# Optimization experiments

Hardware: AMD Instinct MI355X
Metric: run time of the kernel (lower is better)

The kernel has to match this reference:

```python
import jax, jax.numpy as jnp
import numpy as np

D = 128          # hidden_dim
H = 4            # num attention heads (torch default nhead=4 in this module)
DH = D // H
NA = 4096        # author nodes
NP = 100000      # paper nodes
EAP = 500000     # author->paper edges
EPA = 500000     # paper->author edges
DFF = 2048       # TransformerEncoderLayer FFN dim (torch default)
OUT = 16
IN_A = 128
IN_P = 256
EPS = 1e-5


def layer_norm(x, g, b):
    mu = jnp.mean(x, -1, keepdims=True)
    var = jnp.mean((x - mu) ** 2, -1, keepdims=True)
    return (x - mu) / jnp.sqrt(var + EPS) * g + b


def scatter_mean(vals, idx, n):
    # torch_scatter 'mean': empty segments yield 0
    s = jax.ops.segment_sum(vals, idx, num_segments=n)
    c = jax.ops.segment_sum(jnp.ones((vals.shape[0], 1), vals.dtype), idx, num_segments=n)
    return s / jnp.maximum(c, 1.0)


def metapath_layer(x_src, x_dst, src, dst, Wv, bv, Wo, bo, g, b):
    # nn.MultiheadAttention applied per-edge with seq_len=1 (query/key/value are
    # [1, E, D]); softmax over a single key is identically 1, so the attention
    # output is exactly out_proj(v_proj(x_src[src])) -- q/k projections have no
    # effect on the output (and zero gradient).
    v = x_src[src] @ Wv.T + bv            # [E, D] gather + value projection
    attn = v @ Wo.T + bo                  # output projection
    agg = scatter_mean(attn, dst, x_dst.shape[0])
    return layer_norm(agg + x_dst, g, b)


def fusion_layer(x, Wqkv, bqkv, Wo, bo, W1, b1, W2, b2, g1, bt1, g2, bt2):
    # torch TransformerEncoderLayer defaults: post-norm, relu, batch_first=False,
    # so x: [S=NA (seq), M (batch = #metapaths), D].
    S, M, _ = x.shape
    qkv = x @ Wqkv.T + bqkv               # [S, M, 3D]
    q, k, v = jnp.split(qkv, 3, axis=-1)
    q = q.reshape(S, M, H, DH)
    k = k.reshape(S, M, H, DH)
    v = v.reshape(S, M, H, DH)
    scores = jnp.einsum('smhd,tmhd->mhst', q, k) / np.float32(np.sqrt(DH))
    a = jax.nn.softmax(scores, axis=-1)
    ctx = jnp.einsum('mhst,tmhd->smhd', a, v).reshape(S, M, D)
    x = layer_norm(x + ctx @ Wo.T + bo, g1, bt1)
    ff = jax.nn.relu(x @ W1.T + b1) @ W2.T + b2
    return layer_norm(x + ff, g2, bt2)


def setup_inputs() -> dict:
    key = jax.random.key(0)
    ks = iter(jax.random.split(key, 64))
    def nrm(shape, scale=0.02):
        return jax.random.normal(next(ks), shape, dtype=jnp.float32) * scale
    inp = {
        'x_author': jax.random.normal(next(ks), (NA, IN_A), dtype=jnp.float32),
        'x_paper': jax.random.normal(next(ks), (NP, IN_P), dtype=jnp.float32),
        'src_ap': jax.random.randint(next(ks), (EAP,), 0, NA),
        'dst_ap': jax.random.randint(next(ks), (EAP,), 0, NP),
        'src_pa': jax.random.randint(next(ks), (EPA,), 0, NP),
        'dst_pa': jax.random.randint(next(ks), (EPA,), 0, NA),
        'pa_W': nrm((D, IN_A)), 'pa_b': nrm((D,)),
        'pp_W': nrm((D, IN_P)), 'pp_b': nrm((D,)),
        'f_Wqkv': nrm((3 * D, D)), 'f_bqkv': nrm((3 * D,)),
        'f_Wo': nrm((D, D)), 'f_bo': nrm((D,)),
        'f_W1': nrm((DFF, D)), 'f_b1': nrm((DFF,)),
        'f_W2': nrm((D, DFF)), 'f_b2': nrm((D,)),
        'f_g1': jnp.ones((D,), jnp.float32), 'f_bt1': jnp.zeros((D,), jnp.float32),
        'f_g2': jnp.ones((D,), jnp.float32), 'f_bt2': jnp.zeros((D,), jnp.float32),
        'cls_W': nrm((OUT, D)), 'cls_b': nrm((OUT,)),
    }
    for i in range(3):
        inp[f'l{i}_Wv'] = nrm((D, D)); inp[f'l{i}_bv'] = nrm((D,))
        inp[f'l{i}_Wo'] = nrm((D, D)); inp[f'l{i}_bo'] = nrm((D,))
        inp[f'l{i}_g'] = jnp.ones((D,), jnp.float32); inp[f'l{i}_b'] = jnp.zeros((D,), jnp.float32)
    return inp


def reference(x_author, x_paper, src_ap, dst_ap, src_pa, dst_pa,
              pa_W, pa_b, pp_W, pp_b,
              f_Wqkv, f_bqkv, f_Wo, f_bo, f_W1, f_b1, f_W2, f_b2,
              f_g1, f_bt1, f_g2, f_bt2, cls_W, cls_b,
              l0_Wv, l0_bv, l0_Wo, l0_bo, l0_g, l0_b,
              l1_Wv, l1_bv, l1_Wo, l1_bo, l1_g, l1_b,
              l2_Wv, l2_bv, l2_Wo, l2_bo, l2_g, l2_b):
    # project node features to hidden_dim
    ha = x_author @ pa_W.T + pa_b         # [NA, D]
    hp = x_paper @ pp_W.T + pp_b          # [NP, D]
    # metapath 0: paper -> author (one MetapathLayer)
    mp0 = metapath_layer(hp, ha, src_pa, dst_pa, l0_Wv, l0_bv, l0_Wo, l0_bo, l0_g, l0_b)
    # metapath 1: author -> paper -> author (two MetapathLayers)
    t = metapath_layer(ha, hp, src_ap, dst_ap, l1_Wv, l1_bv, l1_Wo, l1_bo, l1_g, l1_b)
    mp1 = metapath_layer(t, ha, src_pa, dst_pa, l2_Wv, l2_bv, l2_Wo, l2_bo, l2_g, l2_b)
    stacked = jnp.stack([mp0, mp1], axis=1)   # [NA, 2, D]
    fused = fusion_layer(stacked, f_Wqkv, f_bqkv, f_Wo, f_bo,
                         f_W1, f_b1, f_W2, f_b2,
                         f_g1, f_bt1, f_g2, f_bt2).mean(axis=1)
    return fused @ cls_W.T + cls_b            # [NA, OUT]
```

## Files before the change

kernel.cpp:

```cpp
#include <hip/hip_runtime.h>
#include <math.h>

constexpr int NA = 4096, NP = 100000, E_AP = 500000, E_PA = 500000;
constexpr int D = 128, DFF = 2048, NOUT = 16, IN_A = 128, IN_P = 256;

typedef __attribute__((ext_vector_type(8))) short bf16x8;
typedef __attribute__((ext_vector_type(4))) float f32x4;
typedef unsigned int u32;

__device__ __forceinline__ ushort f2b(float x) {
    union { float f; unsigned u; } v; v.f = x;
    unsigned r = v.u + 0x7fff + ((v.u >> 16) & 1);
    return (ushort)(r >> 16);
}
__device__ __forceinline__ float b2f(ushort h) {
    union { unsigned u; float f; } v; v.u = (unsigned)h << 16;
    return v.f;
}
__device__ __forceinline__ u32 fbits(float x) {
    union { float f; u32 u; } v; v.f = x; return v.u;
}

__device__ __forceinline__ bf16x8 cvtfrag(float4 a, float4 b) {
    union { u32 w[4]; bf16x8 v; } r;
    asm("v_cvt_pk_bf16_f32 %0, %1, %2" : "=v"(r.w[0]) : "v"(a.x), "v"(a.y));
    asm("v_cvt_pk_bf16_f32 %0, %1, %2" : "=v"(r.w[1]) : "v"(a.z), "v"(a.w));
    asm("v_cvt_pk_bf16_f32 %0, %1, %2" : "=v"(r.w[2]) : "v"(b.x), "v"(b.y));
    asm("v_cvt_pk_bf16_f32 %0, %1, %2" : "=v"(r.w[3]) : "v"(b.z), "v"(b.w));
    return r.v;
}

#define GLL(gp, lp) __builtin_amdgcn_global_load_lds( \
    (const __attribute__((address_space(1))) u32*)(gp), \
    (__attribute__((address_space(3))) u32*)(lp), 16, 0, 0)

#define MFMA16(a, b, c) __builtin_amdgcn_mfma_f32_16x16x32_bf16((a), (b), (c), 0, 0, 0)

__global__ __launch_bounds__(256) void gemm_bf16(
    const ushort* __restrict__ Abf, const float* __restrict__ Af32, int lda,
    const ushort* __restrict__ B, int ldb,
    const float* __restrict__ bias,
    float* __restrict__ outf, ushort* __restrict__ outh, int ldc,
    int M, int N, int K, int act)
{
    __shared__ uint8_t lds[(16 + 32) * 1040];
    uint8_t* sAb = lds;
    uint8_t* sBb = lds + 16 * 1040;

    const int wave = threadIdx.x >> 6;
    const int lane = threadIdx.x & 63;
    const int l16 = lane & 15, quad = lane >> 4;
    const int row0 = blockIdx.y * 64;
    const int col0 = blockIdx.x * 128;
    const int wrg = (wave >> 1) * 2;
    const int wc0 = (wave & 1) * 64;
    const int nz = gridDim.z;
    const int ksub = K / nz;
    const int kbeg = blockIdx.z * ksub;
    const int kgrps = ksub >> 7;

    f32x4 acc[2][4] = {};

    const int sr = lane & 15, sc = lane >> 4;
    const int arow = min(row0 + lane, M - 1);
    const int ag = lane >> 4;
    uint8_t* adst = sAb + (ag * 4 + wave) * 1040 + sr * 16;

    for (int grp = 0; grp < kgrps; ++grp) {
        const int kg = kbeg + grp * 128;
        if (grp) __syncthreads();
        #pragma unroll
        for (int gg = 0; gg < 2; ++gg) {
            int g = wave * 2 + gg;
            const ushort* bp = B + (long)(col0 + g * 16 + sr) * ldb + kg + sc * 8;
            #pragma unroll
            for (int s = 0; s < 4; ++s)
                GLL(bp + s * 32, sBb + (g * 4 + s) * 1040);
        }
        if (Af32) {
            const float* ap = Af32 + (long)arow * lda + kg + wave * 32;
            #pragma unroll
            for (int q = 0; q < 4; ++q) {
                float4 f0 = *(const float4*)(ap + q * 8);
                float4 f1 = *(const float4*)(ap + q * 8 + 4);
                *(bf16x8*)(adst + q * 256) = cvtfrag(f0, f1);
            }
        } else {
            const ushort* ap = Abf + (long)arow * lda + kg + wave * 32;
            #pragma unroll
            for (int q = 0; q < 4; ++q)
                *(bf16x8*)(adst + q * 256) = *(const bf16x8*)(ap + q * 8);
        }
        __syncthreads();
        #pragma unroll
        for (int s = 0; s < 4; ++s) {
            bf16x8 af[2], bfr[4];
            #pragma unroll
            for (int i = 0; i < 2; ++i)
                af[i] = *(const bf16x8*)(sAb + ((wrg + i) * 4 + s) * 1040 + lane * 16);
            #pragma unroll
            for (int j = 0; j < 4; ++j)
                bfr[j] = *(const bf16x8*)(sBb + (((wc0 >> 4) + j) * 4 + s) * 1040 + lane * 16);
            #pragma unroll
            for (int i = 0; i < 2; ++i)
                #pragma unroll
                for (int j = 0; j < 4; ++j)
                    acc[i][j] = MFMA16(af[i], bfr[j], acc[i][j]);
        }
    }

    if (outh && nz == 1) {
        __syncthreads();
        ushort* sC = (ushort*)lds;
        #pragma unroll
        for (int i = 0; i < 2; ++i) {
            #pragma unroll
            for (int r = 0; r < 4; ++r) {
                int lrow = wrg * 16 + i * 16 + quad * 4 + r;
                #pragma unroll
                for (int j = 0; j < 4; ++j) {
                    int lcol = wc0 + j * 16 + l16;
                    float v = acc[i][j][r] + (bias ? bias[col0 + lcol] : 0.f);
                    if (act) v = fmaxf(v, 0.f);
                    sC[lrow * 134 + lcol] = f2b(v);
                }
            }
        }
        __syncthreads();
        int rr = threadIdx.x >> 2, qq = threadIdx.x & 3;
        int grow = row0 + rr;
        if (grow < M) {
            const ushort* src = sC + rr * 134 + qq * 32;
            ushort* dst = outh + (long)grow * ldc + col0 + qq * 32;
            #pragma unroll
            for (int k = 0; k < 4; ++k)
                *(bf16x8*)(dst + k * 8) = *(const bf16x8*)(src + k * 8);
        }
        return;
    }

    #pragma unroll
    for (int i = 0; i < 2; ++i) {
        #pragma unroll
        for (int r = 0; r < 4; ++r) {
            int row = row0 + wrg * 16 + i * 16 + quad * 4 + r;
            if (row >= M) continue;
            #pragma unroll
            for (int j = 0; j < 4; ++j) {
                int col = col0 + wc0 + j * 16 + l16;
                if (nz > 1) {
                    atomicAdd(&outf[(long)row * ldc + col], acc[i][j][r]);
                } else {
                    float v = acc[i][j][r] + (bias ? bias[col] : 0.f);
                    if (act) v = fmaxf(v, 0.f);
                    if (outf) outf[(long)row * ldc + col] = v;
                }
            }
        }
    }
}

__global__ __launch_bounds__(256) void ffn_fused(
    const ushort* __restrict__ x1b,
    const ushort* __restrict__ W1b,
    const ushort* __restrict__ W2b,
    const float* __restrict__ b1,
    float* __restrict__ outf)
{
    __shared__ uint8_t lds[56 * 1040];
    uint8_t* sX  = lds;
    uint8_t* sW1 = lds + 16 * 1040;
    uint8_t* sW2 = lds + 32 * 1040;
    uint8_t* sH  = lds + 48 * 1040;

    const int wave = threadIdx.x >> 6;
    const int lane = threadIdx.x & 63;
    const int l16 = lane & 15, quad = lane >> 4;
    const int sr = lane & 15, sc = lane >> 4;
    const int row0 = blockIdx.x * 64;
    const int dbeg = blockIdx.y * 512;

    const int xg = wave >> 1;
    const int ch = wave & 1;

    {
        const ushort* xp = x1b + (long)(row0 + wave * 16 + sr) * 128 + sc * 8;
        #pragma unroll
        for (int s = 0; s < 4; ++s)
            GLL(xp + s * 32, sX + (wave * 4 + s) * 1040);
    }

    f32x4 acc2[2][4] = {};

    for (int c = 0; c < 8; ++c) {
        const int kc = dbeg + c * 64;
        {
            const ushort* w1p = W1b + (long)(kc + wave * 16 + sr) * 128 + sc * 8;
            #pragma unroll
            for (int s = 0; s < 4; ++s)
                GLL(w1p + s * 32, sW1 + (wave * 4 + s) * 1040);
            #pragma unroll
            for (int gg = 0; gg < 2; ++gg) {
                int cg = wave * 2 + gg;
                const ushort* w2p = W2b + (long)(cg * 16 + sr) * 2048 + kc + sc * 8;
                #pragma unroll
                for (int s2 = 0; s2 < 2; ++s2)
                    GLL(w2p + s2 * 32, sW2 + (cg * 2 + s2) * 1040);
            }
        }
        __syncthreads();

        f32x4 acc1[2][2] = {};
        #pragma unroll
        for (int s = 0; s < 4; ++s) {
            bf16x8 a0 = *(const bf16x8*)(sX + ((xg * 2 + 0) * 4 + s) * 1040 + lane * 16);
            bf16x8 a1 = *(const bf16x8*)(sX + ((xg * 2 + 1) * 4 + s) * 1040 + lane * 16);
            bf16x8 w0 = *(const bf16x8*)(sW1 + ((ch * 2 + 0) * 4 + s) * 1040 + lane * 16);
            bf16x8 w1 = *(const bf16x8*)(sW1 + ((ch * 2 + 1) * 4 + s) * 1040 + lane * 16);
            acc1[0][0] = MFMA16(a0, w0, acc1[0][0]);
            acc1[0][1] = MFMA16(a0, w1, acc1[0][1]);
            acc1[1][0] = MFMA16(a1, w0, acc1[1][0]);
            acc1[1][1] = MFMA16(a1, w1, acc1[1][1]);
        }
        float bb0 = b1[kc + ch * 32 + l16];
        float bb1 = b1[kc + ch * 32 + 16 + l16];
        #pragma unroll
        for (int i = 0; i < 2; ++i) {
            uint8_t* hb = sH + ((xg * 2 + i) * 2 + ch) * 1040;
            #pragma unroll
            for (int j = 0; j < 2; ++j) {
                float bb = j ? bb1 : bb0;
                int q = ((j * 16 + l16) >> 3) & 3;
                int byo = (l16 & 7) * 2;
                #pragma unroll
                for (int r = 0; r < 4; ++r) {
                    float v = fmaxf(acc1[i][j][r] + bb, 0.f);
                    *(ushort*)(hb + q * 256 + (quad * 4 + r) * 16 + byo) = f2b(v);
                }
            }
        }
        __syncthreads();

        #pragma unroll
        for (int s2 = 0; s2 < 2; ++s2) {
            bf16x8 h0 = *(const bf16x8*)(sH + ((xg * 2 + 0) * 2 + s2) * 1040 + lane * 16);
            bf16x8 h1 = *(const bf16x8*)(sH + ((xg * 2 + 1) * 2 + s2) * 1040 + lane * 16);
            #pragma unroll
            for (int j2 = 0; j2 < 4; ++j2) {
                bf16x8 wb = *(const bf16x8*)(sW2 + ((ch * 4 + j2) * 2 + s2) * 1040 + lane * 16);
                acc2[0][j2] = MFMA16(h0, wb, acc2[0][j2]);
                acc2[1][j2] = MFMA16(h1, wb, acc2[1][j2]);
            }
        }
        __syncthreads();
    }

    #pragma unroll
    for (int i = 0; i < 2; ++i)
        #pragma unroll
        for (int r = 0; r < 4; ++r) {
            int row = row0 + xg * 32 + i * 16 + quad * 4 + r;
            #pragma unroll
            for (int j2 = 0; j2 < 4; ++j2) {
                int col = ch * 64 + j2 * 16 + l16;
                atomicAdd(&outf[(long)row * 128 + col], acc2[i][j2][r]);
            }
        }
}

__global__ __launch_bounds__(256) void fuse_weights(
    const float* __restrict__ Wv0, const float* __restrict__ bv0,
    const float* __restrict__ Wo0, const float* __restrict__ bo0,
    const float* __restrict__ Wv1, const float* __restrict__ bv1,
    const float* __restrict__ Wo1, const float* __restrict__ bo1,
    const float* __restrict__ Wv2, const float* __restrict__ bv2,
    const float* __restrict__ Wo2, const float* __restrict__ bo2,
    ushort* __restrict__ Wfb, float* __restrict__ beff)
{
    int blk = blockIdx.x;
    if (blk >= 192) {
        int l = blk - 192;
        const float* bv = l == 0 ? bv0 : (l == 1 ? bv1 : bv2);
        const float* Wo = l == 0 ? Wo0 : (l == 1 ? Wo1 : Wo2);
        const float* bo = l == 0 ? bo0 : (l == 1 ? bo1 : bo2);
        if (threadIdx.x < 128) {
            int r = threadIdx.x;
            float acc = bo[r];
            #pragma unroll 8
            for (int j = 0; j < 128; ++j) acc += Wo[r * 128 + j] * bv[j];
            beff[l * 128 + r] = acc;
        }
        return;
    }
    int l = blk >> 6;
    const float* Wv = l == 0 ? Wv0 : (l == 1 ? Wv1 : Wv2);
    const float* Wo = l == 0 ? Wo0 : (l == 1 ? Wo1 : Wo2);
    int r = (blk & 63) * 2 + (threadIdx.x >> 7);
    int c = threadIdx.x & 127;
    float acc = 0.f;
    #pragma unroll 8
    for (int j = 0; j < 128; ++j)
        acc += Wo[r * 128 + j] * Wv[j * 128 + c];
    Wfb[l * 16384 + r * 128 + c] = f2b(acc);
}

__global__ void hist2(const int* __restrict__ dA, int* __restrict__ cA,
                      const int* __restrict__ dP, int* __restrict__ cP, int E)
{
    int e = blockIdx.x * 256 + threadIdx.x;
    if (e >= E) return;
    if (blockIdx.y == 0) atomicAdd(&cA[dA[e]], 1);
    else                 atomicAdd(&cP[dP[e]], 1);
}

__global__ __launch_bounds__(256) void scan_local2(
    const int* __restrict__ inA, int* __restrict__ outA, int* __restrict__ bsumA, int nA,
    const int* __restrict__ inP, int* __restrict__ outP, int* __restrict__ bsumP, int nP)
{
    const int* in  = blockIdx.y ? inP  : inA;
    int* out       = blockIdx.y ? outP : outA;
    int* bsum      = blockIdx.y ? bsumP : bsumA;
    int n          = blockIdx.y ? nP : nA;
    __shared__ int wsum[4];
    int t = threadIdx.x;
    int base = blockIdx.x * 1024 + t * 4;
    int v0 = (base + 0 < n) ? in[base + 0] : 0;
    int v1 = (base + 1 < n) ? in[base + 1] : 0;
    int v2 = (base + 2 < n) ? in[base + 2] : 0;
    int v3 = (base + 3 < n) ? in[base + 3] : 0;
    int tsum = v0 + v1 + v2 + v3;
    int lane = t & 63;
    int x = tsum;
    #pragma unroll
    for (int o = 1; o < 64; o <<= 1) {
        int y = __shfl_up(x, o, 64);
        if (lane >= o) x += y;
    }
    int wid = t >> 6;
    if (lane == 63) wsum[wid] = x;
    __syncthreads();
    int woff = 0;
    #pragma unroll
    for (int ww = 0; ww < 3; ++ww) if (ww < wid) woff += wsum[ww];
    int excl = x - tsum + woff;
    if (base + 0 < n) out[base + 0] = excl;
    if (base + 1 < n) out[base + 1] = excl + v0;
    if (base + 2 < n) out[base + 2] = excl + v0 + v1;
    if (base + 3 < n) out[base + 3] = excl + v0 + v1 + v2;
    if (bsum && t == 255) bsum[blockIdx.x] = excl + tsum;
}

__global__ void scan_add2(int* __restrict__ offA, const int* __restrict__ bA,
                          int* __restrict__ curA, int nA,
                          int* __restrict__ offP, const int* __restrict__ bP,
                          int* __restrict__ curP, int nP)
{
    int* off       = blockIdx.y ? offP : offA;
    const int* bofs= blockIdx.y ? bP   : bA;
    int* cur       = blockIdx.y ? curP : curA;
    int n          = blockIdx.y ? nP : nA;
    int i = blockIdx.x * 256 + threadIdx.x;
    if (i < n) {
        int v = off[i] + bofs[i >> 10];
        off[i] = v;
        cur[i] = v;
    }
}

__global__ void fill2(const int* __restrict__ sA, const int* __restrict__ dA,
                      int* __restrict__ cuA, int* __restrict__ eA,
                      const int* __restrict__ sP, const int* __restrict__ dP,
                      int* __restrict__ cuP, int* __restrict__ eP, int E)
{
    int e = blockIdx.x * 256 + threadIdx.x;
    if (e >= E) return;
    if (blockIdx.y == 0) { int slot = atomicAdd(&cuA[dA[e]], 1); eA[slot] = sA[e]; }
    else                 { int slot = atomicAdd(&cuP[dP[e]], 1); eP[slot] = sP[e]; }
}

__global__ __launch_bounds__(256) void gather_sum(
    const ushort* __restrict__ z, const int* __restrict__ off,
    const int* __restrict__ cnt, const int* __restrict__ esrc,
    float* __restrict__ outf, int R)
{
    int grp = threadIdx.x >> 5;
    int tg  = threadIdx.x & 31;
    int gid = blockIdx.x * 8 + grp;
    int row = gid >> 2, chunk = gid & 3;
    if (row >= R) return;
    int e0 = off[row], deg = cnt[row];
    int c0 = e0 + (int)(((long)deg * chunk) >> 2);
    int c1 = e0 + (int)(((long)deg * (chunk + 1)) >> 2);
    if (c0 >= c1) return;
    float a0 = 0.f, a1 = 0.f, a2 = 0.f, a3 = 0.f;
    int e = c0;
    for (; e + 4 <= c1; e += 4) {
        int s0 = esrc[e], s1 = esrc[e + 1], s2 = esrc[e + 2], s3 = esrc[e + 3];
        ushort4 v0 = ((const ushort4*)(z + (long)s0 * 128))[tg];
        ushort4 v1 = ((const ushort4*)(z + (long)s1 * 128))[tg];
        ushort4 v2 = ((const ushort4*)(z + (long)s2 * 128))[tg];
        ushort4 v3 = ((const ushort4*)(z + (long)s3 * 128))[tg];
        a0 += b2f(v0.x) + b2f(v1.x) + b2f(v2.x) + b2f(v3.x);
        a1 += b2f(v0.y) + b2f(v1.y) + b2f(v2.y) + b2f(v3.y);
        a2 += b2f(v0.z) + b2f(v1.z) + b2f(v2.z) + b2f(v3.z);
        a3 += b2f(v0.w) + b2f(v1.w) + b2f(v2.w) + b2f(v3.w);
    }
    for (; e < c1; ++e) {
        int s = esrc[e];
        ushort4 v = ((const ushort4*)(z + (long)s * 128))[tg];
        a0 += b2f(v.x); a1 += b2f(v.y); a2 += b2f(v.z); a3 += b2f(v.w);
    }
    float* op = outf + (long)row * 128 + tg * 4;
    atomicAdd(op + 0, a0); atomicAdd(op + 1, a1);
    atomicAdd(op + 2, a2); atomicAdd(op + 3, a3);
}

__global__ __launch_bounds__(256) void gather_mean_ln(
    const ushort* __restrict__ z, const int* __restrict__ off,
    const int* __restrict__ cnt, const int* __restrict__ esrc,
    const ushort* __restrict__ base, const float* __restrict__ g,
    const float* __restrict__ b, ushort* __restrict__ outh, int R)
{
    int grp = threadIdx.x >> 5;
    int tg  = threadIdx.x & 31;
    int row = blockIdx.x * 8 + grp;
    if (row >= R) return;
    int e0 = off[row], deg = cnt[row];
    int eend = e0 + deg;
    float a0 = 0.f, a1 = 0.f, a2 = 0.f, a3 = 0.f;
    int e = e0;
    for (; e + 4 <= eend; e += 4) {
        int s0 = esrc[e], s1 = esrc[e + 1], s2 = esrc[e + 2], s3 = esrc[e + 3];
        ushort4 v0 = ((const ushort4*)(z + (long)s0 * 128))[tg];
        ushort4 v1 = ((const ushort4*)(z + (long)s1 * 128))[tg];
        ushort4 v2 = ((const ushort4*)(z + (long)s2 * 128))[tg];
        ushort4 v3 = ((const ushort4*)(z + (long)s3 * 128))[tg];
        a0 += b2f(v0.x) + b2f(v1.x) + b2f(v2.x) + b2f(v3.x);
        a1 += b2f(v0.y) + b2f(v1.y) + b2f(v2.y) + b2f(v3.y);
        a2 += b2f(v0.z) + b2f(v1.z) + b2f(v2.z) + b2f(v3.z);
        a3 += b2f(v0.w) + b2f(v1.w) + b2f(v2.w) + b2f(v3.w);
    }
    for (; e < eend; ++e) {
        int s = esrc[e];
        ushort4 v = ((const ushort4*)(z + (long)s * 128))[tg];
        a0 += b2f(v.x); a1 += b2f(v.y); a2 += b2f(v.z); a3 += b2f(v.w);
    }
    float inv = 1.f / fmaxf((float)deg, 1.f);
    ushort4 bs = ((const ushort4*)(base + (long)row * 128))[tg];
    float x0 = a0 * inv + b2f(bs.x), x1 = a1 * inv + b2f(bs.y);
    float x2 = a2 * inv + b2f(bs.z), x3 = a3 * inv + b2f(bs.w);
    float s1 = x0 + x1 + x2 + x3;
    #pragma unroll
    for (int o = 1; o < 32; o <<= 1) s1 += __shfl_xor(s1, o, 64);
    float mu = s1 * (1.f / 128.f);
    float d0 = x0 - mu, d1 = x1 - mu, d2 = x2 - mu, d3 = x3 - mu;
    float s2 = d0 * d0 + d1 * d1 + d2 * d2 + d3 * d3;
    #pragma unroll
    for (int o = 1; o < 32; o <<= 1) s2 += __shfl_xor(s2, o, 64);
    float rstd = rsqrtf(s2 * (1.f / 128.f) + 1e-5f);
    float4 gv = ((const float4*)g)[tg];
    float4 bv = ((const float4*)b)[tg];
    ushort4 h4;
    h4.x = f2b(d0 * rstd * gv.x + bv.x);
    h4.y = f2b(d1 * rstd * gv.y + bv.y);
    h4.z = f2b(d2 * rstd * gv.z + bv.z);
    h4.w = f2b(d3 * rstd * gv.w + bv.w);
    ((ushort4*)(outh + (long)row * 128))[tg] = h4;
}

__global__ __launch_bounds__(128) void mean_add_ln(
    const float* __restrict__ a, const float* __restrict__ bias,
    const float* __restrict__ basef, const ushort* __restrict__ baseh,
    const float* __restrict__ g, const float* __restrict__ b,
    float* __restrict__ outf, ushort* __restrict__ outh, int out_ld, int R,
    const int* __restrict__ degp)
{
    int row = blockIdx.x;
    if (row >= R) return;
    int d = threadIdx.x;
    float x = a[(long)row * 128 + d];
    if (degp) x *= 1.f / fmaxf((float)degp[row], 1.f);
    if (bias) x += bias[d];
    if (basef) x += basef[(long)row * 128 + d];
    if (baseh) x += b2f(baseh[(long)row * 128 + d]);

    __shared__ float red[4];
    float s = x;
    #pragma unroll
    for (int o = 32; o >= 1; o >>= 1) s += __shfl_xor(s, o, 64);
    if ((d & 63) == 0) red[d >> 6] = s;
    __syncthreads();
    float mu = (red[0] + red[1]) * (1.f / 128.f);
    float dx = x - mu;
    float s2 = dx * dx;
    #pragma unroll
    for (int o = 32; o >= 1; o >>= 1) s2 += __shfl_xor(s2, o, 64);
    if ((d & 63) == 0) red[2 + (d >> 6)] = s2;
    __syncthreads();
    float var = (red[2] + red[3]) * (1.f / 128.f);
    float v = dx * rsqrtf(var + 1e-5f) * g[d] + b[d];
    if (outf) outf[(long)row * out_ld + d] = v;
    if (outh) outh[(long)row * out_ld + d] = f2b(v);
}

struct CvtArgs { const float* in[6]; ushort* out[6]; int n4[6]; };
__global__ void cvt_multi(CvtArgs a)
{
    int j = blockIdx.y;
    int i = blockIdx.x * 256 + threadIdx.x;
    if (i >= a.n4[j]) return;
    float4 v = ((const float4*)a.in[j])[i];
    ushort4 o;
    o.x = f2b(v.x); o.y = f2b(v.y); o.z = f2b(v.z); o.w = f2b(v.w);
    ((ushort4*)a.out[j])[i] = o;
}

__global__ __launch_bounds__(256) void flash_attn(
    const ushort* __restrict__ qkvb,
    float* __restrict__ opart, float* __restrict__ lpart_g)
{
    const int qt = blockIdx.x;
    const int mh = blockIdx.y;
    const int ks = blockIdx.z;
    const int m = mh >> 2, h = mh & 3;
    const int wave = threadIdx.x >> 6;
    const int lane = threadIdx.x & 63;
    const int l16 = lane & 15, quad = lane >> 4;

    __shared__ ushort sK[2][64 * 40];
    __shared__ u32    sV[2][32 * 32];
    __shared__ u32    sP[4][16 * 32];

    const int q0 = qt * 64 + wave * 16;
    const float qs = 0.17677669529663687f * 1.4426950408889634f;
    bf16x8 qf;
    {
        bf16x8 qraw = *(const bf16x8*)(qkvb + ((long)(q0 + l16) * 2 + m) * 384 + h * 32 + quad * 8);
        #pragma unroll
        for (int j = 0; j < 8; ++j)
            qf[j] = (short)f2b(b2f((ushort)qraw[j]) * qs);
    }

    f32x4 oacc0 = {0.f, 0.f, 0.f, 0.f};
    f32x4 oacc1 = {0.f, 0.f, 0.f, 0.f};
    float lp = 0.f;

    const int skey = threadIdx.x >> 2, sseg = threadIdx.x & 3;
    const int vkp  = threadIdx.x & 31, vdc  = (threadIdx.x >> 5) * 4;
    const int kbeg = ks * (NA / 2);
    const ushort* kbase = qkvb + ((long)((kbeg + skey) * 2 + m)) * 384 + 128 + h * 32 + sseg * 8;
    const ushort* vbase = qkvb + ((long)((kbeg + vkp * 2) * 2 + m)) * 384 + 256 + h * 32 + vdc;
    const int kwo = skey * 40 + sseg * 8;
    int vwo[4];
    #pragma unroll
    for (int i = 0; i < 4; ++i)
        vwo[i] = (vdc + i) * 32 + ((((vkp >> 2) ^ ((vdc + i) & 7)) << 2) | (vkp & 3));

    bf16x8 kreg = *(const bf16x8*)(kbase);
    ushort4 v0r = *(const ushort4*)(vbase);
    ushort4 v1r = *(const ushort4*)(vbase + 768);
    *(bf16x8*)(&sK[0][kwo]) = kreg;
    sV[0][vwo[0]] = (u32)v0r.x | ((u32)v1r.x << 16);
    sV[0][vwo[1]] = (u32)v0r.y | ((u32)v1r.y << 16);
    sV[0][vwo[2]] = (u32)v0r.z | ((u32)v1r.z << 16);
    sV[0][vwo[3]] = (u32)v0r.w | ((u32)v1r.w << 16);
    __syncthreads();

    int cur = 0;
    for (int kt = 0; kt < 32; ++kt) {
        const bool more = (kt + 1) < 32;
        if (more) {
            long off = (long)(kt + 1) * 64 * 768;
            kreg = *(const bf16x8*)(kbase + off);
            v0r  = *(const ushort4*)(vbase + off);
            v1r  = *(const ushort4*)(vbase + off + 768);
        }

        #pragma unroll
        for (int t = 0; t < 4; ++t) {
            bf16x8 kf = *(const bf16x8*)(&sK[cur][(t * 16 + l16) * 40 + quad * 8]);
            f32x4 s = {0.f, 0.f, 0.f, 0.f};
            s = MFMA16(kf, qf, s);
            float p0 = exp2f(s[0]), p1 = exp2f(s[1]);
            float p2 = exp2f(s[2]), p3 = exp2f(s[3]);
            lp += (p0 + p1) + (p2 + p3);
            u32 lo = __builtin_amdgcn_perm(fbits(p1), fbits(p0), 0x07060302u);
            u32 hi = __builtin_amdgcn_perm(fbits(p3), fbits(p2), 0x07060302u);
            u32* dst = &sP[wave][l16 * 32 +
                                 ((((t * 2 + (quad >> 1)) ^ (l16 & 7)) << 2) | ((quad & 1) * 2))];
            dst[0] = lo; dst[1] = hi;
        }
        #pragma unroll
        for (int c = 0; c < 2; ++c) {
            const int gp = ((c * 4 + quad) ^ (l16 & 7)) << 2;
            bf16x8 pf  = *(const bf16x8*)(&sP[wave][l16 * 32 + gp]);
            bf16x8 vf0 = *(const bf16x8*)(&sV[cur][l16 * 32 + gp]);
            bf16x8 vf1 = *(const bf16x8*)(&sV[cur][(16 + l16) * 32 + gp]);
            oacc0 = MFMA16(pf, vf0, oacc0);
            oacc1 = MFMA16(pf, vf1, oacc1);
        }

        if (more) {
            const int nxt = cur ^ 1;
            *(bf16x8*)(&sK[nxt][kwo]) = kreg;
            sV[nxt][vwo[0]] = (u32)v0r.x | ((u32)v1r.x << 16);
            sV[nxt][vwo[1]] = (u32)v0r.y | ((u32)v1r.y << 16);
            sV[nxt][vwo[2]] = (u32)v0r.z | ((u32)v1r.z << 16);
            sV[nxt][vwo[3]] = (u32)v0r.w | ((u32)v1r.w << 16);
            __syncthreads();
            cur = nxt;
        }
    }

    lp += __shfl_xor(lp, 16, 64);
    lp += __shfl_xor(lp, 32, 64);
    if (quad == 0)
        lpart_g[(long)(mh * 2 + ks) * NA + q0 + l16] = lp;

    #pragma unroll
    for (int r = 0; r < 4; ++r) {
        int qr = q0 + quad * 4 + r;
        long ob = ((long)(mh * 2 + ks) * NA + qr) * 32;
        opart[ob + l16]      = oacc0[r];
        opart[ob + 16 + l16] = oacc1[r];
    }
}

__global__ void attn_combine(const float* __restrict__ opart,
                             const float* __restrict__ lpart,
                             ushort* __restrict__ ctxb)
{
    int idx = blockIdx.x * 256 + threadIdx.x;
    int d = idx & 31;
    int row = idx >> 5;
    int mh = row >> 12, qrow = row & 4095;
    float o = 0.f, l = 0.f;
    #pragma unroll
    for (int ks = 0; ks < 2; ++ks) {
        long rb = (long)(mh * 2 + ks) * NA + qrow;
        o += opart[rb * 32 + d];
        l += lpart[rb];
    }
    int m = mh >> 2, h = mh & 3;
    ctxb[((long)qrow * 2 + m) * 128 + h * 32 + d] = f2b(o / l);
}

__global__ void classify_kernel(const float* __restrict__ x2,
                                const float* __restrict__ Wc,
                                const float* __restrict__ bc,
                                float* __restrict__ out)
{
    int idx = blockIdx.x * 256 + threadIdx.x;
    int a2 = idx >> 4, o = idx & 15;
    const float* r0 = x2 + (long)(a2 * 2) * 128;
    const float* r1 = r0 + 128;
    const float* w = Wc + o * 128;
    float acc = bc[o];
    #pragma unroll 4
    for (int dd = 0; dd < 128; ++dd) acc += 0.5f * (r0[dd] + r1[dd]) * w[dd];
    out[idx] = acc;
}

static void bgemm(hipStream_t st, const ushort* Abf, const float* Af32, int lda,
                  const ushort* B, int ldb,
                  const float* bias, float* outf, ushort* outh, int ldc,
                  int M, int N, int K, int act = 0, int ksplit = 1)
{
    dim3 grid(N / 128, (M + 63) / 64, ksplit);
    gemm_bf16<<<grid, 256, 0, st>>>(Abf, Af32, lda, B, ldb, bias, outf, outh,
                                    ldc, M, N, K, act);
}

extern "C" void kernel_launch(void* const* d_in, const int* in_sizes, int n_in,
                              void* d_out, int out_size, void* d_ws, size_t ws_size,
                              hipStream_t stream)
{
    const float* x_author = (const float*)d_in[0];
    const float* x_paper  = (const float*)d_in[1];
    const int*   src_ap   = (const int*)d_in[2];
    const int*   dst_ap   = (const int*)d_in[3];
    const int*   src_pa   = (const int*)d_in[4];
    const int*   dst_pa   = (const int*)d_in[5];
    const float* pa_W = (const float*)d_in[6];   const float* pa_b = (const float*)d_in[7];
    const float* pp_W = (const float*)d_in[8];   const float* pp_b = (const float*)d_in[9];
    const float* f_Wqkv = (const float*)d_in[10]; const float* f_bqkv = (const float*)d_in[11];
    const float* f_Wo = (const float*)d_in[12];  const float* f_bo = (const float*)d_in[13];
    const float* f_W1 = (const float*)d_in[14];  const float* f_b1 = (const float*)d_in[15];
    const float* f_W2 = (const float*)d_in[16];  const float* f_b2 = (const float*)d_in[17];
    const float* f_g1 = (const float*)d_in[18];  const float* f_bt1 = (const float*)d_in[19];
    const float* f_g2 = (const float*)d_in[20];  const float* f_bt2 = (const float*)d_in[21];
    const float* cls_W = (const float*)d_in[22]; const float* cls_b = (const float*)d_in[23];
    const float* l0_Wv = (const float*)d_in[24]; const float* l0_bv = (const float*)d_in[25];
    const float* l0_Wo = (const float*)d_in[26]; const float* l0_bo = (const float*)d_in[27];
    const float* l0_g  = (const float*)d_in[28]; const float* l0_b  = (const float*)d_in[29];
    const float* l1_Wv = (const float*)d_in[30]; const float* l1_bv = (const float*)d_in[31];
    const float* l1_Wo = (const float*)d_in[32]; const float* l1_bo = (const float*)d_in[33];
    const float* l1_g  = (const float*)d_in[34]; const float* l1_b  = (const float*)d_in[35];
    const float* l2_Wv = (const float*)d_in[36]; const float* l2_bv = (const float*)d_in[37];
    const float* l2_Wo = (const float*)d_in[38]; const float* l2_bo = (const float*)d_in[39];
    const float* l2_g  = (const float*)d_in[40]; const float* l2_b  = (const float*)d_in[41];

    uint8_t* w = (uint8_t*)d_ws;
    ushort* TB  = (ushort*)(w + 0);
    float*  OPART = (float*)(w + 26214400);
    float*  LPART = (float*)(w + 43515904);
    ushort* HPB = (ushort*)(w + 61440000);
    ushort* ZB  = (ushort*)(w + 87040000);
    uint8_t* p2 = w + 102400000;
    ushort* QKVB = (ushort*)(p2 + 0);
    ushort* CTXB = (ushort*)(p2 + 6291456);
    float*  TMP  = (float*)(p2 + 8388608);
    float*  GMA32= (float*)(p2 + 8388608);
    float*  X1   = (float*)(p2 + 12582912);
    ushort* X1B  = (ushort*)(p2 + 16777216);
    float*  TMP2 = (float*)(p2 + 18874368);
    float*  X2   = (float*)(p2 + 23068672);
    uint8_t* tail = p2 + 27262976;
    ushort* STKB  = (ushort*)(tail + 4194304);
    ushort* HAB   = (ushort*)(tail + 6291456);
    ushort* WFB   = (ushort*)(tail + 8388608);
    ushort* PAWB  = (ushort*)(tail + 8486912);
    ushort* PPWB  = (ushort*)(tail + 8519680);
    ushort* WQKVB = (ushort*)(tail + 8585216);
    ushort* WOB   = (ushort*)(tail + 8683520);
    ushort* W1B   = (ushort*)(tail + 8716288);
    ushort* W2B   = (ushort*)(tail + 9240576);
    float*  BEFF  = (float*)(tail + 9764864);
    int*   CNT_A  = (int*)(tail + 9766400);
    int*   OFF_A  = (int*)(tail + 9782784);
    int*   CUR_A  = (int*)(tail + 9799168);
    int*   CNT_P  = (int*)(tail + 9815552);
    int*   OFF_P  = (int*)(tail + 10215552);
    int*   CUR_P  = (int*)(tail + 10615552);
    int*   ESRC_PA= (int*)(tail + 11015552);
    int*   ESRC_AP= (int*)(tail + 13015552);
    int*   BSUM_A = (int*)(tail + 15015552);
    int*   BSUM_P = (int*)(tail + 15016576);
    float* TMPA   = (float*)(tail + 15017984);

    CvtArgs ca;
    ca.in[0] = pa_W;   ca.out[0] = PAWB;  ca.n4[0] = D * IN_A / 4;
    ca.in[1] = pp_W;   ca.out[1] = PPWB;  ca.n4[1] = D * IN_P / 4;
    ca.in[2] = f_Wqkv; ca.out[2] = WQKVB; ca.n4[2] = 3 * D * D / 4;
    ca.in[3] = f_Wo;   ca.out[3] = WOB;   ca.n4[3] = D * D / 4;
    ca.in[4] = f_W1;   ca.out[4] = W1B;   ca.n4[4] = DFF * D / 4;
    ca.in[5] = f_W2;   ca.out[5] = W2B;   ca.n4[5] = D * DFF / 4;
    cvt_multi<<<dim3((DFF * D / 4 + 255) / 256, 6), 256, 0, stream>>>(ca);

    fuse_weights<<<195, 256, 0, stream>>>(l0_Wv, l0_bv, l0_Wo, l0_bo,
                                          l1_Wv, l1_bv, l1_Wo, l1_bo,
                                          l2_Wv, l2_bv, l2_Wo, l2_bo, WFB, BEFF);

    hipMemsetAsync(CNT_A, 0, (size_t)NA * 4, stream);
    hipMemsetAsync(CNT_P, 0, (size_t)NP * 4, stream);
    const int nbA = (NA + 1023) / 1024, nbP = (NP + 1023) / 1024;
    hist2<<<dim3((E_PA + 255) / 256, 2), 256, 0, stream>>>(dst_pa, CNT_A, dst_ap, CNT_P, E_PA);
    scan_local2<<<dim3(nbP, 2), 256, 0, stream>>>(CNT_A, OFF_A, BSUM_A, NA,
                                                  CNT_P, OFF_P, BSUM_P, NP);
    scan_local2<<<dim3(1, 2), 256, 0, stream>>>(BSUM_A, BSUM_A, nullptr, nbA,
                                                BSUM_P, BSUM_P, nullptr, nbP);
    scan_add2<<<dim3((NP + 255) / 256, 2), 256, 0, stream>>>(OFF_A, BSUM_A, CUR_A, NA,
                                                             OFF_P, BSUM_P, CUR_P, NP);
    fill2<<<dim3((E_PA + 255) / 256, 2), 256, 0, stream>>>(
        src_pa, dst_pa, CUR_A, ESRC_PA, src_ap, dst_ap, CUR_P, ESRC_AP, E_PA);

    bgemm(stream, nullptr, x_author, IN_A, PAWB, IN_A, pa_b, nullptr, HAB, D, NA, D, IN_A);
    bgemm(stream, nullptr, x_paper,  IN_P, PPWB, IN_P, pp_b, nullptr, HPB, D, NP, D, IN_P);

    hipMemsetAsync(GMA32, 0, (size_t)NA * D * 4, stream);
    gather_sum<<<(NA * 4 + 7) / 8, 256, 0, stream>>>(HPB, OFF_A, CNT_A, ESRC_PA, GMA32, NA);
    bgemm(stream, nullptr, GMA32, D, WFB, D, nullptr, TMPA, nullptr, D, NA, D, D);
    mean_add_ln<<<NA, 128, 0, stream>>>(TMPA, BEFF, nullptr, HAB, l0_g, l0_b,
                                        nullptr, STKB, 256, NA, CNT_A);

    bgemm(stream, HAB, nullptr, D, WFB + 16384, D, BEFF + 128, nullptr, ZB, D, NA, D, D);
    gather_mean_ln<<<(NP + 7) / 8, 256, 0, stream>>>(
        ZB, OFF_P, CNT_P, ESRC_AP, HPB, l1_g, l1_b, TB, NP);

    hipMemsetAsync(GMA32, 0, (size_t)NA * D * 4, stream);
    gather_sum<<<(NA * 4 + 7) / 8, 256, 0, stream>>>(TB, OFF_A, CNT_A, ESRC_PA, GMA32, NA);
    bgemm(stream, nullptr, GMA32, D, WFB + 32768, D, nullptr, TMPA, nullptr, D, NA, D, D);
    mean_add_ln<<<NA, 128, 0, stream>>>(TMPA, BEFF + 256, nullptr, HAB, l2_g, l2_b,
                                        nullptr, STKB + 128, 256, NA, CNT_A);

    bgemm(stream, STKB, nullptr, D, WQKVB, D, f_bqkv, nullptr, QKVB, 3 * D, 2 * NA, 3 * D, D);
    flash_attn<<<dim3(NA / 64, 8, 2), 256, 0, stream>>>(QKVB, OPART, LPART);
    attn_combine<<<8 * NA * 32 / 256, 256, 0, stream>>>(OPART, LPART, CTXB);

    bgemm(stream, CTXB, nullptr, D, WOB, D, f_bo, TMP, nullptr, D, 2 * NA, D, D);
    mean_add_ln<<<2 * NA, 128, 0, stream>>>(TMP, nullptr, nullptr, STKB, f_g1, f_bt1,
                                            X1, X1B, 128, 2 * NA, nullptr);

    hipMemsetAsync(TMP2, 0, (size_t)2 * NA * D * 4, stream);
    ffn_fused<<<dim3(2 * NA / 64, 4), 256, 0, stream>>>(X1B, W1B, W2B, f_b1, TMP2);
    mean_add_ln<<<2 * NA, 128, 0, stream>>>(TMP2, f_b2, X1, nullptr, f_g2, f_bt2,
                                            X2, nullptr, 128, 2 * NA, nullptr);

    classify_kernel<<<(NA * NOUT) / 256, 256, 0, stream>>>(X2, cls_W, cls_b, (float*)d_out);
}
```

Baseline: 701.7 us.

## Record per-edge slots in histogram and compute author means before projection

```diff
diff --git a/kernel.cpp b/kernel.cpp
--- a/kernel.cpp
+++ b/kernel.cpp
@@ -304,13 +304,14 @@
     Wfb[l * 16384 + r * 128 + c] = f2b(acc);
 }
 
-__global__ void hist2(const int* __restrict__ dA, int* __restrict__ cA,
-                      const int* __restrict__ dP, int* __restrict__ cP, int E)
+__global__ void hist2(const int* __restrict__ dA, int* __restrict__ cA, int* __restrict__ lA,
+                      const int* __restrict__ dP, int* __restrict__ cP, int* __restrict__ lP,
+                      int E)
 {
     int e = blockIdx.x * 256 + threadIdx.x;
     if (e >= E) return;
-    if (blockIdx.y == 0) atomicAdd(&cA[dA[e]], 1);
-    else                 atomicAdd(&cP[dP[e]], 1);
+    if (blockIdx.y == 0) lA[e] = atomicAdd(&cA[dA[e]], 1);
+    else                 lP[e] = atomicAdd(&cP[dP[e]], 1);
 }
 
 __global__ __launch_bounds__(256) void scan_local2(
@@ -350,76 +351,33 @@
     if (bsum && t == 255) bsum[blockIdx.x] = excl + tsum;
 }
 
-__global__ void scan_add2(int* __restrict__ offA, const int* __restrict__ bA,
-                          int* __restrict__ curA, int nA,
-                          int* __restrict__ offP, const int* __restrict__ bP,
-                          int* __restrict__ curP, int nP)
+__global__ void scan_add2(int* __restrict__ offA, const int* __restrict__ bA, int nA,
+                          int* __restrict__ offP, const int* __restrict__ bP, int nP)
 {
     int* off       = blockIdx.y ? offP : offA;
     const int* bofs= blockIdx.y ? bP   : bA;
-    int* cur       = blockIdx.y ? curP : curA;
     int n          = blockIdx.y ? nP : nA;
     int i = blockIdx.x * 256 + threadIdx.x;
-    if (i < n) {
-        int v = off[i] + bofs[i >> 10];
-        off[i] = v;
-        cur[i] = v;
-    }
+    if (i < n) off[i] += bofs[i >> 10];
 }
 
 __global__ void fill2(const int* __restrict__ sA, const int* __restrict__ dA,
-                      int* __restrict__ cuA, int* __restrict__ eA,
+                      const int* __restrict__ oA, const int* __restrict__ lA,
+                      int* __restrict__ eA,
                       const int* __restrict__ sP, const int* __restrict__ dP,
-                      int* __restrict__ cuP, int* __restrict__ eP, int E)
+                      const int* __restrict__ oP, const int* __restrict__ lP,
+                      int* __restrict__ eP, int E)
 {
     int e = blockIdx.x * 256 + threadIdx.x;
     if (e >= E) return;
-    if (blockIdx.y == 0) { int slot = atomicAdd(&cuA[dA[e]], 1); eA[slot] = sA[e]; }
-    else                 { int slot = atomicAdd(&cuP[dP[e]], 1); eP[slot] = sP[e]; }
-}
-
-__global__ __launch_bounds__(256) void gather_sum(
+    if (blockIdx.y == 0) eA[oA[dA[e]] + lA[e]] = sA[e];
+    else                 eP[oP[dP[e]] + lP[e]] = sP[e];
+}
+
+__global__ __launch_bounds__(256) void gather_mean(
     const ushort* __restrict__ z, const int* __restrict__ off,
     const int* __restrict__ cnt, const int* __restrict__ esrc,
-    float* __restrict__ outf, int R)
-{
-    int grp = threadIdx.x >> 5;
-    int tg  = threadIdx.x & 31;
-    int gid = blockIdx.x * 8 + grp;
-    int row = gid >> 2, chunk = gid & 3;
-    if (row >= R) return;
-    int e0 = off[row], deg = cnt[row];
-    int c0 = e0 + (int)(((long)deg * chunk) >> 2);
-    int c1 = e0 + (int)(((long)deg * (chunk + 1)) >> 2);
-    if (c0 >= c1) return;
-    float a0 = 0.f, a1 = 0.f, a2 = 0.f, a3 = 0.f;
-    int e = c0;
-    for (; e + 4 <= c1; e += 4) {
-        int s0 = esrc[e], s1 = esrc[e + 1], s2 = esrc[e + 2], s3 = esrc[e + 3];
-        ushort4 v0 = ((const ushort4*)(z + (long)s0 * 128))[tg];
-        ushort4 v1 = ((const ushort4*)(z + (long)s1 * 128))[tg];
-        ushort4 v2 = ((const ushort4*)(z + (long)s2 * 128))[tg];
-        ushort4 v3 = ((const ushort4*)(z + (long)s3 * 128))[tg];
-        a0 += b2f(v0.x) + b2f(v1.x) + b2f(v2.x) + b2f(v3.x);
-        a1 += b2f(v0.y) + b2f(v1.y) + b2f(v2.y) + b2f(v3.y);
-        a2 += b2f(v0.z) + b2f(v1.z) + b2f(v2.z) + b2f(v3.z);
-        a3 += b2f(v0.w) + b2f(v1.w) + b2f(v2.w) + b2f(v3.w);
-    }
-    for (; e < c1; ++e) {
-        int s = esrc[e];
-        ushort4 v = ((const ushort4*)(z + (long)s * 128))[tg];
-        a0 += b2f(v.x); a1 += b2f(v.y); a2 += b2f(v.z); a3 += b2f(v.w);
-    }
-    float* op = outf + (long)row * 128 + tg * 4;
-    atomicAdd(op + 0, a0); atomicAdd(op + 1, a1);
-    atomicAdd(op + 2, a2); atomicAdd(op + 3, a3);
-}
-
-__global__ __launch_bounds__(256) void gather_mean_ln(
-    const ushort* __restrict__ z, const int* __restrict__ off,
-    const int* __restrict__ cnt, const int* __restrict__ esrc,
-    const ushort* __restrict__ base, const float* __restrict__ g,
-    const float* __restrict__ b, ushort* __restrict__ outh, int R)
+    ushort* __restrict__ outh, int R)
 {
     int grp = threadIdx.x >> 5;
     int tg  = threadIdx.x & 31;
@@ -446,6 +404,41 @@
         a0 += b2f(v.x); a1 += b2f(v.y); a2 += b2f(v.z); a3 += b2f(v.w);
     }
     float inv = 1.f / fmaxf((float)deg, 1.f);
+    ushort4 h4 = {f2b(a0 * inv), f2b(a1 * inv), f2b(a2 * inv), f2b(a3 * inv)};
+    ((ushort4*)(outh + (long)row * 128))[tg] = h4;
+}
+
+__global__ __launch_bounds__(256) void gather_mean_ln(
+    const ushort* __restrict__ z, const int* __restrict__ off,
+    const int* __restrict__ cnt, const int* __restrict__ esrc,
+    const ushort* __restrict__ base, const float* __restrict__ g,
+    const float* __restrict__ b, ushort* __restrict__ outh, int R)
+{
+    int grp = threadIdx.x >> 5;
+    int tg  = threadIdx.x & 31;
+    int row = blockIdx.x * 8 + grp;
+    if (row >= R) return;
+    int e0 = off[row], deg = cnt[row];
+    int eend = e0 + deg;
+    float a0 = 0.f, a1 = 0.f, a2 = 0.f, a3 = 0.f;
+    int e = e0;
+    for (; e + 4 <= eend; e += 4) {
+        int s0 = esrc[e], s1 = esrc[e + 1], s2 = esrc[e + 2], s3 = esrc[e + 3];
+        ushort4 v0 = ((const ushort4*)(z + (long)s0 * 128))[tg];
+        ushort4 v1 = ((const ushort4*)(z + (long)s1 * 128))[tg];
+        ushort4 v2 = ((const ushort4*)(z + (long)s2 * 128))[tg];
+        ushort4 v3 = ((const ushort4*)(z + (long)s3 * 128))[tg];
+        a0 += b2f(v0.x) + b2f(v1.x) + b2f(v2.x) + b2f(v3.x);
+        a1 += b2f(v0.y) + b2f(v1.y) + b2f(v2.y) + b2f(v3.y);
+        a2 += b2f(v0.z) + b2f(v1.z) + b2f(v2.z) + b2f(v3.z);
+        a3 += b2f(v0.w) + b2f(v1.w) + b2f(v2.w) + b2f(v3.w);
+    }
+    for (; e < eend; ++e) {
+        int s = esrc[e];
+        ushort4 v = ((const ushort4*)(z + (long)s * 128))[tg];
+        a0 += b2f(v.x); a1 += b2f(v.y); a2 += b2f(v.z); a3 += b2f(v.w);
+    }
+    float inv = 1.f / fmaxf((float)deg, 1.f);
     ushort4 bs = ((const ushort4*)(base + (long)row * 128))[tg];
     float x0 = a0 * inv + b2f(bs.x), x1 = a1 * inv + b2f(bs.y);
     float x2 = a2 * inv + b2f(bs.z), x3 = a3 * inv + b2f(bs.w);
@@ -472,14 +465,12 @@
     const float* __restrict__ a, const float* __restrict__ bias,
     const float* __restrict__ basef, const ushort* __restrict__ baseh,
     const float* __restrict__ g, const float* __restrict__ b,
-    float* __restrict__ outf, ushort* __restrict__ outh, int out_ld, int R,
-    const int* __restrict__ degp)
+    float* __restrict__ outf, ushort* __restrict__ outh, int out_ld, int R)
 {
     int row = blockIdx.x;
     if (row >= R) return;
     int d = threadIdx.x;
     float x = a[(long)row * 128 + d];
-    if (degp) x *= 1.f / fmaxf((float)degp[row], 1.f);
     if (bias) x += bias[d];
     if (basef) x += basef[(long)row * 128 + d];
     if (baseh) x += b2f(baseh[(long)row * 128 + d]);
@@ -704,13 +695,14 @@
     ushort* TB  = (ushort*)(w + 0);
     float*  OPART = (float*)(w + 26214400);
     float*  LPART = (float*)(w + 43515904);
+    int*   LOC_A  = (int*)(w + 44040192);
+    int*   LOC_P  = (int*)(w + 46140416);
     ushort* HPB = (ushort*)(w + 61440000);
     ushort* ZB  = (ushort*)(w + 87040000);
     uint8_t* p2 = w + 102400000;
     ushort* QKVB = (ushort*)(p2 + 0);
     ushort* CTXB = (ushort*)(p2 + 6291456);
     float*  TMP  = (float*)(p2 + 8388608);
-    float*  GMA32= (float*)(p2 + 8388608);
     float*  X1   = (float*)(p2 + 12582912);
     ushort* X1B  = (ushort*)(p2 + 16777216);
     float*  TMP2 = (float*)(p2 + 18874368);
@@ -718,6 +710,7 @@
     uint8_t* tail = p2 + 27262976;
     ushort* STKB  = (ushort*)(tail + 4194304);
     ushort* HAB   = (ushort*)(tail + 6291456);
+    ushort* GMA   = (ushort*)(tail + 7340032);
     ushort* WFB   = (ushort*)(tail + 8388608);
     ushort* PAWB  = (ushort*)(tail + 8486912);
     ushort* PPWB  = (ushort*)(tail + 8519680);
@@ -728,10 +721,8 @@
     float*  BEFF  = (float*)(tail + 9764864);
     int*   CNT_A  = (int*)(tail + 9766400);
     int*   OFF_A  = (int*)(tail + 9782784);
-    int*   CUR_A  = (int*)(tail + 9799168);
     int*   CNT_P  = (int*)(tail + 9815552);
     int*   OFF_P  = (int*)(tail + 10215552);
-    int*   CUR_P  = (int*)(tail + 10615552);
     int*   ESRC_PA= (int*)(tail + 11015552);
     int*   ESRC_AP= (int*)(tail + 13015552);
     int*   BSUM_A = (int*)(tail + 15015552);
@@ -754,34 +745,34 @@
     hipMemsetAsync(CNT_A, 0, (size_t)NA * 4, stream);
     hipMemsetAsync(CNT_P, 0, (size_t)NP * 4, stream);
     const int nbA = (NA + 1023) / 1024, nbP = (NP + 1023) / 1024;
-    hist2<<<dim3((E_PA + 255) / 256, 2), 256, 0, stream>>>(dst_pa, CNT_A, dst_ap, CNT_P, E_PA);
+    hist2<<<dim3((E_PA + 255) / 256, 2), 256, 0, stream>>>(
+        dst_pa, CNT_A, LOC_A, dst_ap, CNT_P, LOC_P, E_PA);
     scan_local2<<<dim3(nbP, 2), 256, 0, stream>>>(CNT_A, OFF_A, BSUM_A, NA,
                                                   CNT_P, OFF_P, BSUM_P, NP);
     scan_local2<<<dim3(1, 2), 256, 0, stream>>>(BSUM_A, BSUM_A, nullptr, nbA,
                                                 BSUM_P, BSUM_P, nullptr, nbP);
-    scan_add2<<<dim3((NP + 255) / 256, 2), 256, 0, stream>>>(OFF_A, BSUM_A, CUR_A, NA,
-                                                             OFF_P, BSUM_P, CUR_P, NP);
+    scan_add2<<<dim3((NP + 255) / 256, 2), 256, 0, stream>>>(OFF_A, BSUM_A, NA,
+                                                             OFF_P, BSUM_P, NP);
     fill2<<<dim3((E_PA + 255) / 256, 2), 256, 0, stream>>>(
-        src_pa, dst_pa, CUR_A, ESRC_PA, src_ap, dst_ap, CUR_P, ESRC_AP, E_PA);
+        src_pa, dst_pa, OFF_A, LOC_A, ESRC_PA,
+        src_ap, dst_ap, OFF_P, LOC_P, ESRC_AP, E_PA);
 
     bgemm(stream, nullptr, x_author, IN_A, PAWB, IN_A, pa_b, nullptr, HAB, D, NA, D, IN_A);
     bgemm(stream, nullptr, x_paper,  IN_P, PPWB, IN_P, pp_b, nullptr, HPB, D, NP, D, IN_P);
 
-    hipMemsetAsync(GMA32, 0, (size_t)NA * D * 4, stream);
-    gather_sum<<<(NA * 4 + 7) / 8, 256, 0, stream>>>(HPB, OFF_A, CNT_A, ESRC_PA, GMA32, NA);
-    bgemm(stream, nullptr, GMA32, D, WFB, D, nullptr, TMPA, nullptr, D, NA, D, D);
-    mean_add_ln<<<NA, 128, 0, stream>>>(TMPA, BEFF, nullptr, HAB, l0_g, l0_b,
-                                        nullptr, STKB, 256, NA, CNT_A);
+    gather_mean<<<(NA + 7) / 8, 256, 0, stream>>>(HPB, OFF_A, CNT_A, ESRC_PA, GMA, NA);
+    bgemm(stream, GMA, nullptr, D, WFB, D, BEFF, TMPA, nullptr, D, NA, D, D);
+    mean_add_ln<<<NA, 128, 0, stream>>>(TMPA, nullptr, nullptr, HAB, l0_g, l0_b,
+                                        nullptr, STKB, 256, NA);
 
     bgemm(stream, HAB, nullptr, D, WFB + 16384, D, BEFF + 128, nullptr, ZB, D, NA, D, D);
     gather_mean_ln<<<(NP + 7) / 8, 256, 0, stream>>>(
         ZB, OFF_P, CNT_P, ESRC_AP, HPB, l1_g, l1_b, TB, NP);
 
-    hipMemsetAsync(GMA32, 0, (size_t)NA * D * 4, stream);
-    gather_sum<<<(NA * 4 + 7) / 8, 256, 0, stream>>>(TB, OFF_A, CNT_A, ESRC_PA, GMA32, NA);
-    bgemm(stream, nullptr, GMA32, D, WFB + 32768, D, nullptr, TMPA, nullptr, D, NA, D, D);
-    mean_add_ln<<<NA, 128, 0, stream>>>(TMPA, BEFF + 256, nullptr, HAB, l2_g, l2_b,
-                                        nullptr, STKB + 128, 256, NA, CNT_A);
+    gather_mean<<<(NA + 7) / 8, 256, 0, stream>>>(TB, OFF_A, CNT_A, ESRC_PA, GMA, NA);
+    bgemm(stream, GMA, nullptr, D, WFB + 32768, D, BEFF + 256, TMPA, nullptr, D, NA, D, D);
+    mean_add_ln<<<NA, 128, 0, stream>>>(TMPA, nullptr, nullptr, HAB, l2_g, l2_b,
+                                        nullptr, STKB + 128, 256, NA);
 
     bgemm(stream, STKB, nullptr, D, WQKVB, D, f_bqkv, nullptr, QKVB, 3 * D, 2 * NA, 3 * D, D);
     flash_attn<<<dim3(NA / 64, 8, 2), 256, 0, stream>>>(QKVB, OPART, LPART);
@@ -789,12 +780,12 @@
 
     bgemm(stream, CTXB, nullptr, D, WOB, D, f_bo, TMP, nullptr, D, 2 * NA, D, D);
     mean_add_ln<<<2 * NA, 128, 0, stream>>>(TMP, nullptr, nullptr, STKB, f_g1, f_bt1,
-                                            X1, X1B, 128, 2 * NA, nullptr);
+                                            X1, X1B, 128, 2 * NA);
 
     hipMemsetAsync(TMP2, 0, (size_t)2 * NA * D * 4, stream);
     ffn_fused<<<dim3(2 * NA / 64, 4), 256, 0, stream>>>(X1B, W1B, W2B, f_b1, TMP2);
     mean_add_ln<<<2 * NA, 128, 0, stream>>>(TMP2, f_b2, X1, nullptr, f_g2, f_bt2,
-                                            X2, nullptr, 128, 2 * NA, nullptr);
+                                            X2, nullptr, 128, 2 * NA);
 
     classify_kernel<<<(NA * NOUT) / 256, 256, 0, stream>>>(X2, cls_W, cls_b, (float*)d_out);
 }
```

Measured after the change: 611.2 us, median of 2. 12.9% less time.
